# Kernel tuning notes

Measured on AMD Instinct MI355X. Metric: run time of the kernel, lower is better.

Reference implementation:

```python
import jax, jax.numpy as jnp
from jax import lax
import numpy as np

N = 4096      # graph nodes
K = 16        # sampled local-neighborhood size (2-hop proxy)
T = 16        # number of templates
NT = 16       # nodes per template
D = 128       # node feature dim
OUTER = 3     # proximal / mirror-descent iterations
INNER = 5     # sinkhorn iterations per outer step
EPS_REL = 0.1 # entropic reg relative to cost range
TINY = 1e-16


def setup_inputs() -> dict:
    key = jax.random.key(0)
    ks = jax.random.split(key, 8)
    x = jax.random.normal(ks[0], (N, D), jnp.float32)
    adj = (jax.random.uniform(ks[1], (N, N)) < 0.004).astype(jnp.float32)
    adj = jnp.maximum(adj, adj.T)
    neighbors = jax.random.randint(ks[2], (N, K), 0, N, dtype=jnp.int32)
    templates = (jax.random.randint(ks[3], (T, NT, NT), 0, 2).astype(jnp.float32)
                 + 0.01 * jax.random.normal(ks[4], (T, NT, NT), jnp.float32))
    templates_features = 0.0012 + 0.02 * jax.random.normal(ks[5], (T, NT, D), jnp.float32)
    q0 = jax.random.uniform(ks[6], (T, NT), jnp.float32)
    alpha0 = jnp.zeros((1,), jnp.float32)
    return {"x": x, "adj": adj, "neighbors": neighbors, "templates": templates,
            "templates_features": templates_features, "q0": q0, "alpha0": alpha0}


def _ltfgw(x, adj, neighbors, templates, templates_features, q0, alpha0):
    n, d = x.shape
    t, nt, _ = templates.shape
    k1 = neighbors.shape[1] + 1
    nb = jnp.concatenate([jnp.arange(n, dtype=neighbors.dtype)[:, None], neighbors], axis=1)  # [N,K1]
    Fi = x[nb]                                    # [N,K1,D] local node features
    C1 = adj[nb[:, :, None], nb[:, None, :]]      # [N,K1,K1] local structure
    C2 = templates                                # [T,NT,NT]
    alpha = jax.nn.sigmoid(alpha0[0])
    q = jax.nn.softmax(q0, axis=1)                # [T,NT] template node weights
    p = jnp.full((k1,), 1.0 / k1, x.dtype)        # uniform local weights
    # squared-euclidean feature cost M: [N,T,K1,NT]
    M = (jnp.sum(Fi**2, -1)[:, None, :, None]
         + jnp.sum(templates_features**2, -1)[None, :, None, :]
         - 2.0 * jnp.einsum('nkd,tmd->ntkm', Fi, templates_features))
    # constant part of squared-loss GW cost
    cC = (jnp.einsum('nij,j->ni', C1**2, p)[:, None, :, None]
          + jnp.einsum('tm,tlm->tl', q, C2**2)[None, :, None, :])
    G0 = jnp.broadcast_to(p[None, None, :, None] * q[None, :, None, :], (n, t, k1, nt))

    def outer_step(G, _):
        gw_grad = cC - 2.0 * jnp.einsum('nij,ntjm,tlm->ntil', C1, G, C2)
        grad = (1.0 - alpha) * M + alpha * gw_grad
        lo = jnp.min(grad, axis=(-2, -1), keepdims=True)
        hi = jnp.max(grad, axis=(-2, -1), keepdims=True)
        eps = EPS_REL * (hi - lo) + TINY
        Kmat = jnp.exp(-(grad - lo) / eps)        # per-(n,t) shift leaves plan invariant

        def sink(uv, _):
            u, v = uv
            u = p[None, None, :] / jnp.maximum(jnp.einsum('ntkm,ntm->ntk', Kmat, v), TINY)
            v = q[None] / jnp.maximum(jnp.einsum('ntkm,ntk->ntm', Kmat, u), TINY)
            return (u, v), None

        u0 = jnp.ones((n, t, k1), x.dtype)
        v0 = jnp.ones((n, t, nt), x.dtype)
        (u, v), _ = lax.scan(sink, (u0, v0), None, length=INNER)
        return u[..., None] * Kmat * v[..., None, :], None

    G, _ = lax.scan(outer_step, G0, None, length=OUTER)
    gw = cC - 2.0 * jnp.einsum('nij,ntjm,tlm->ntil', C1, G, C2)
    # fused GW distance of every node's local graph to every template: [N,T]
    return jnp.sum(((1.0 - alpha) * M + alpha * gw) * G, axis=(-2, -1))


def reference(x, adj, neighbors, templates, templates_features, q0, alpha0):
    return _ltfgw(x, adj, neighbors, templates, templates_features, q0, alpha0)
```

## Files before the change

### kernel.cpp

```cpp
#include <hip/hip_runtime.h>
#include <math.h>


#define NN 4096
#define KNB 16
#define K1 17
#define C1STRIDE 20
#define C1NODE 340
#define TSTR 296
#define TINYF 1e-16f

typedef const __attribute__((address_space(4))) float* c4fp;
typedef const __attribute__((address_space(4))) int*   c4ip;
__device__ __forceinline__ float sload(const float* p){ return *(c4fp)(unsigned long long)p; }
__device__ __forceinline__ int   sloadi(const int* p) { return *(c4ip)(unsigned long long)p; }

template<int CTRL>
__device__ __forceinline__ float dppmov(float x) {
  return __int_as_float(
      __builtin_amdgcn_update_dpp(0, __float_as_int(x), CTRL, 0xF, 0xF, true));
}
__device__ __forceinline__ float xor4v(float x) {
  return dppmov<0x1B>(dppmov<0x141>(x));
}
__device__ __forceinline__ float rsum16(float x) {
  x += dppmov<0xB1>(x); x += dppmov<0x4E>(x);
  x += xor4v(x);        x += dppmov<0x128>(x);
  return x;
}
__device__ __forceinline__ float rmin16(float x) {
  x = fminf(x, dppmov<0xB1>(x)); x = fminf(x, dppmov<0x4E>(x));
  x = fminf(x, xor4v(x));        x = fminf(x, dppmov<0x128>(x));
  return x;
}
__device__ __forceinline__ float rmax16(float x) {
  x = fmaxf(x, dppmov<0xB1>(x)); x = fmaxf(x, dppmov<0x4E>(x));
  x = fmaxf(x, xor4v(x));        x = fmaxf(x, dppmov<0x128>(x));
  return x;
}
__device__ __forceinline__ float rcpn(float x) {
  float r = __builtin_amdgcn_rcpf(x);
  return r * (2.f - x * r);
}

#define WSTEP(C, R) { g = dppmov<C>(g); acc = fmaf(g, c2reg[R], acc); }
#define WALK15() \
  WSTEP(0xB1,1)  WSTEP(0x1B,2)  WSTEP(0xB1,3)  WSTEP(0x141,4) \
  WSTEP(0xB1,5)  WSTEP(0x1B,6)  WSTEP(0xB1,7)  WSTEP(0x140,8) \
  WSTEP(0xB1,9)  WSTEP(0x1B,10) WSTEP(0xB1,11) WSTEP(0x141,12) \
  WSTEP(0xB1,13) WSTEP(0x1B,14) WSTEP(0xB1,15)

#define PG_GEMM  256
#define PG_XSQ   (PG_GEMM + 1024)
#define PG_SCAL  PG_XSQ
#define PG_C1    (PG_SCAL + 1)
#define PG_TOT   (PG_C1 + 4096)

__global__ __launch_bounds__(256) void prep_combined(
    const float* __restrict__ x, const float* __restrict__ adj,
    const int* __restrict__ neighbors, const float* __restrict__ templates_,
    const float* __restrict__ tf, const float* __restrict__ q0,
    const float* __restrict__ alpha0,
    float* __restrict__ P, float* __restrict__ C1ws, float* __restrict__ xsq,
    float* __restrict__ tfsq, float* __restrict__ qmat, float* __restrict__ cq,
    float* __restrict__ walpha) {
  __shared__ __align__(16) float smem[2 * 64 * 68];
  const int b = blockIdx.x, tid = threadIdx.x;

  if (b < PG_GEMM) {
    float (*As)[68] = (float (*)[68])smem;
    float (*Bs)[68] = (float (*)[68])(smem + 64 * 68);
    int tx = tid & 15, ty = tid >> 4;
    int r0 = (b & 63) * 64, c0 = (b >> 6) * 64;
    float acc[4][4] = {};
    for (int h = 0; h < 2; ++h) {
      __syncthreads();
#pragma unroll
      for (int q = 0; q < 4; ++q) {
        int f = tid + 256*q;
        int row = f >> 4, d4 = (f & 15) << 2;
        float4 a = *(const float4*)&x[(r0+row)*128 + h*64 + d4];
        As[d4+0][row]=a.x; As[d4+1][row]=a.y; As[d4+2][row]=a.z; As[d4+3][row]=a.w;
        float4 bb = *(const float4*)&tf[(c0+row)*128 + h*64 + d4];
        Bs[d4+0][row]=bb.x; Bs[d4+1][row]=bb.y; Bs[d4+2][row]=bb.z; Bs[d4+3][row]=bb.w;
      }
      __syncthreads();
#pragma unroll
      for (int d = 0; d < 64; ++d) {
        float4 a = *(const float4*)&As[d][ty*4];
        float4 bb = *(const float4*)&Bs[d][tx*4];
        float av[4]={a.x,a.y,a.z,a.w}, bv[4]={bb.x,bb.y,bb.z,bb.w};
#pragma unroll
        for (int i = 0; i < 4; ++i)
#pragma unroll
          for (int j = 0; j < 4; ++j) acc[i][j] = fmaf(av[i], bv[j], acc[i][j]);
      }
    }
#pragma unroll
    for (int i = 0; i < 4; ++i) {
      float4 o; o.x=acc[i][0]; o.y=acc[i][1]; o.z=acc[i][2]; o.w=acc[i][3];
      *(float4*)&P[(r0 + ty*4 + i)*256 + c0 + tx*4] = o;
    }
    return;
  }

  if (b < PG_XSQ) {
    int n = (b - PG_GEMM)*4 + (tid >> 6), lane = tid & 63;
    float2 v = *(const float2*)&x[n*128 + lane*2];
    float s = fmaf(v.x, v.x, v.y*v.y);
    s += __shfl_xor(s,1); s += __shfl_xor(s,2);  s += __shfl_xor(s,4);
    s += __shfl_xor(s,8); s += __shfl_xor(s,16); s += __shfl_xor(s,32);
    if (lane == 0) xsq[n] = s;
    return;
  }

  if (b == PG_SCAL) {
    int t = tid >> 4, l = tid & 15;
    if (tid == 0) walpha[0] = 1.f / (1.f + expf(-alpha0[0]));
    float qr[16]; float mx = -3.0e38f;
#pragma unroll
    for (int m = 0; m < 16; ++m) { qr[m] = q0[t*16+m]; mx = fmaxf(mx, qr[m]); }
    float s = 0.f;
#pragma unroll
    for (int m = 0; m < 16; ++m) { qr[m] = expf(qr[m]-mx); s += qr[m]; }
    float inv = 1.f / s;
    qmat[tid] = qr[l] * inv;
    float c = 0.f;
#pragma unroll
    for (int m = 0; m < 16; ++m) {
      float c2 = templates_[t*256 + l*16 + m];
      c = fmaf(qr[m]*inv, c2*c2, c);
    }
    cq[tid] = c;
    float ts = 0.f;
#pragma unroll
    for (int dq = 0; dq < 32; ++dq) {
      float4 v = *(const float4*)&tf[tid*128 + dq*4];
      ts = fmaf(v.x,v.x,ts); ts = fmaf(v.y,v.y,ts);
      ts = fmaf(v.z,v.z,ts); ts = fmaf(v.w,v.w,ts);
    }
    tfsq[tid] = ts;
    return;
  }

  {
    int n = b - PG_C1;
    int*   nbs  = (int*)smem;
    float* c1sh = smem + 32;
    if (tid < K1) nbs[tid] = (tid == 0) ? n : neighbors[n*KNB + tid - 1];
    __syncthreads();
    for (int e = tid; e < 289; e += 256) {
      int i = e / 17, j = e % 17;
      float v = adj[nbs[i]*NN + nbs[j]];
      C1ws[n*C1NODE + i*C1STRIDE + j] = v;
      c1sh[e] = v;
    }
    __syncthreads();
    bool nz = false;
    if (tid < K1) {
      float s = 0.f;
#pragma unroll
      for (int j = 0; j < K1; ++j) {
        float v = c1sh[tid*17 + j];
        s = fmaf(v, v, s); nz |= (v != 0.f);
      }
      C1ws[n*C1NODE + tid*C1STRIDE + 17] = s * (1.f/17.f);
    }
    unsigned long long bal = __ballot(nz);
    if (tid == 0)
      ((int*)C1ws)[n*C1NODE + 18] = (int)(bal & 0x1FFFF);
  }
}

__global__ __launch_bounds__(256, 2) void ltfgw_main(
    const float* __restrict__ P, const float* __restrict__ C1ws,
    const float* __restrict__ xsq, const float* __restrict__ tfsq,
    const float* __restrict__ qmat, const float* __restrict__ cq,
    const float* __restrict__ walpha, const int* __restrict__ neighbors,
    const float* __restrict__ templates_, float* __restrict__ out) {
  __shared__ __align__(16) float Ksh[16 * TSTR];
  __shared__ __align__(16) float Ush[256];
  __shared__ __align__(16) float Vsh[256];

  const int tid = threadIdx.x;
  const int t = tid >> 4, l = tid & 15;
  const int n = blockIdx.x;

  const float alpha = sload(walpha);
  const float oma = 1.f - alpha;
  const float na2 = -2.f * alpha;
  const int mask = sloadi((const int*)C1ws + n*C1NODE + 18);

  int nbk[K1];
  nbk[0] = n;
#pragma unroll
  for (int k = 1; k < K1; ++k) nbk[k] = sloadi(neighbors + n*KNB + (k-1));

  const float tfsq_l = tfsq[tid];
  const float cq_l   = cq[tid];
  const float q_l    = qmat[tid];

  float Mcol[K1];
#pragma unroll
  for (int k = 0; k < K1; ++k) {
    float xs  = sload(xsq + nbk[k]);
    float cc1 = sload(C1ws + n*C1NODE + k*C1STRIDE + 17);
    float pv  = P[nbk[k]*256 + tid];
    Mcol[k] = oma * (xs + tfsq_l - 2.f*pv) + alpha * (cc1 + cq_l);
  }

  float c2reg[16];
#pragma unroll
  for (int r = 0; r < 16; ++r)
    c2reg[r] = na2 * templates_[t*256 + l*16 + (l ^ r)];

  float Gcol[K1];
#pragma unroll
  for (int j = 0; j < K1; ++j) Gcol[j] = (1.f/17.f) * q_l;

  const int tb = t * TSTR;
  float ur[16], u16 = 0.f, vm = 1.f;

#pragma unroll 1
  for (int outer = 0; outer < 3; ++outer) {
    float Kc[K1];
    float lo = 3.0e38f, hi = -3.0e38f;
#pragma unroll
    for (int i = 0; i < K1; ++i) {
      float gr = Mcol[i];
      if (mask & (1 << i)) {
        const float* c1r = C1ws + n*C1NODE + i*C1STRIDE;
        float s = 0.f;
#pragma unroll
        for (int j = 0; j < K1; ++j) s = fmaf(sload(c1r + j), Gcol[j], s);
        float g = s, acc = s * c2reg[0];
        WALK15()
        gr += acc;
      }
      Kc[i] = gr;
      lo = fminf(lo, gr); hi = fmaxf(hi, gr);
    }
    lo = rmin16(lo); hi = rmax16(hi);
    float eps = 0.1f * (hi - lo) + TINYF;
    float sc = 1.4426950408889634f * __builtin_amdgcn_rcpf(eps);
    float nsc = -sc, losc = lo * sc;
#pragma unroll
    for (int i = 0; i < K1; ++i) {
      Kc[i] = __builtin_amdgcn_exp2f(fmaf(Kc[i], nsc, losc));
      Ksh[tb + i*17 + l] = Kc[i];
    }
    float Krow[16];
#pragma unroll
    for (int jq = 0; jq < 4; ++jq) {
      float4 v = *(const float4*)&Ksh[tb + l*17 + jq*4];
      Krow[jq*4+0]=v.x; Krow[jq*4+1]=v.y; Krow[jq*4+2]=v.z; Krow[jq*4+3]=v.w;
    }

    float vlane = 1.f;
    Vsh[tid] = 1.f;
#pragma unroll 1
    for (int it = 0; it < 5; ++it) {
      float vr[16];
#pragma unroll
      for (int q = 0; q < 4; ++q) {
        float4 v = *(const float4*)&Vsh[t*16 + q*4];
        vr[q*4+0]=v.x; vr[q*4+1]=v.y; vr[q*4+2]=v.z; vr[q*4+3]=v.w;
      }
      float w = 0.f;
#pragma unroll
      for (int j = 0; j < 16; ++j) w = fmaf(Krow[j], vr[j], w);
      float w16 = rsum16(Kc[16] * vlane);
      float um = (1.f/17.f) * rcpn(fmaxf(w,   TINYF));
      u16      = (1.f/17.f) * rcpn(fmaxf(w16, TINYF));
      Ush[tid] = um;
#pragma unroll
      for (int q = 0; q < 4; ++q) {
        float4 v = *(const float4*)&Ush[t*16 + q*4];
        ur[q*4+0]=v.x; ur[q*4+1]=v.y; ur[q*4+2]=v.z; ur[q*4+3]=v.w;
      }
      float sg = u16 * Kc[16];
#pragma unroll
      for (int k = 0; k < 16; ++k) sg = fmaf(ur[k], Kc[k], sg);
      vlane = q_l * rcpn(fmaxf(sg, TINYF));
      Vsh[tid] = vlane;
    }
    vm = vlane;
#pragma unroll
    for (int k = 0; k < 16; ++k) Gcol[k] = ur[k] * Kc[k] * vm;
    Gcol[16] = u16 * Kc[16] * vm;
  }

  float acc1 = 0.f;
#pragma unroll
  for (int i = 0; i < K1; ++i) acc1 = fmaf(Mcol[i], Gcol[i], acc1);
#pragma unroll
  for (int i = 0; i < K1; ++i) {
    if (mask & (1 << i)) {
      const float* c1r = C1ws + n*C1NODE + i*C1STRIDE;
      float s = 0.f;
#pragma unroll
      for (int j = 0; j < K1; ++j) s = fmaf(sload(c1r + j), Gcol[j], s);
      float g = s, acc = s * c2reg[0];
      WALK15()
      acc1 = fmaf(acc, Gcol[i], acc1);
    }
  }
  float accout = rsum16(acc1);
  if (l == 0) out[n*16 + t] = accout;
}

extern "C" void kernel_launch(void* const* d_in, const int* in_sizes, int n_in,
                              void* d_out, int out_size, void* d_ws, size_t ws_size,
                              hipStream_t stream) {
  const float* x          = (const float*)d_in[0];
  const float* adj        = (const float*)d_in[1];
  const int*   neighbors  = (const int*)  d_in[2];
  const float* templates_ = (const float*)d_in[3];
  const float* tfeat      = (const float*)d_in[4];
  const float* q0         = (const float*)d_in[5];
  const float* alpha0     = (const float*)d_in[6];
  float* out = (float*)d_out;

  float* ws     = (float*)d_ws;
  float* P      = ws;
  float* C1ws   = P + 4096*256;
  float* xsq    = C1ws + 4096*C1NODE;
  float* tfsq   = xsq + 4096;
  float* qmat   = tfsq + 256;
  float* cq     = qmat + 256;
  float* walpha = cq + 256;

  hipLaunchKernelGGL(prep_combined, dim3(PG_TOT), dim3(256), 0, stream,
                     x, adj, neighbors, templates_, tfeat, q0, alpha0,
                     P, C1ws, xsq, tfsq, qmat, cq, walpha);
  hipLaunchKernelGGL(ltfgw_main, dim3(4096), dim3(256), 0, stream,
                     P, C1ws, xsq, tfsq, qmat, cq, walpha, neighbors,
                     templates_, out);
}
```

Baseline: 181.1 us.

## Bit-pack adjacency matrix and gather local structure from packed bits

Adds a streaming pass that converts the dense float adjacency into a bitmask via wave ballots. The per-node C1 gather now runs as a separate kernel that reads bits instead of scattered floats. The intent is to replace latency-bound random reads of a 64 MB matrix with one coalesced sweep plus cache-friendly gathers from an 8x smaller array. It adds a kernel launch and a full read of adj. The exp argument is also computed with a sub/mul instead of a precomputed FMA.

```diff
diff --git a/kernel.cpp b/kernel.cpp
--- a/kernel.cpp
+++ b/kernel.cpp
@@ -51,18 +51,18 @@
   WSTEP(0xB1,13) WSTEP(0x1B,14) WSTEP(0xB1,15)
 
 #define PG_GEMM  256
-#define PG_XSQ   (PG_GEMM + 1024)
+#define PG_PACK  (PG_GEMM + 1024)
+#define PG_XSQ   (PG_PACK + 1024)
 #define PG_SCAL  PG_XSQ
-#define PG_C1    (PG_SCAL + 1)
-#define PG_TOT   (PG_C1 + 4096)
+#define PG_TOT   (PG_SCAL + 1)
 
 __global__ __launch_bounds__(256) void prep_combined(
     const float* __restrict__ x, const float* __restrict__ adj,
-    const int* __restrict__ neighbors, const float* __restrict__ templates_,
-    const float* __restrict__ tf, const float* __restrict__ q0,
-    const float* __restrict__ alpha0,
-    float* __restrict__ P, float* __restrict__ C1ws, float* __restrict__ xsq,
-    float* __restrict__ tfsq, float* __restrict__ qmat, float* __restrict__ cq,
+    const float* __restrict__ templates_, const float* __restrict__ tf,
+    const float* __restrict__ q0, const float* __restrict__ alpha0,
+    float* __restrict__ P, unsigned long long* __restrict__ pk,
+    float* __restrict__ xsq, float* __restrict__ tfsq,
+    float* __restrict__ qmat, float* __restrict__ cq,
     float* __restrict__ walpha) {
   __shared__ __align__(16) float smem[2 * 64 * 68];
   const int b = blockIdx.x, tid = threadIdx.x;
@@ -104,8 +104,21 @@
     return;
   }
 
+  if (b < PG_PACK) {
+    int wave = (b - PG_GEMM)*4 + (tid >> 6);
+    int lane = tid & 63;
+#pragma unroll 4
+    for (int it = 0; it < 64; ++it) {
+      int w64 = wave + it*4096;
+      float v = adj[(size_t)w64*64 + lane];
+      unsigned long long m = __ballot(v != 0.f);
+      if (lane == 0) pk[w64] = m;
+    }
+    return;
+  }
+
   if (b < PG_XSQ) {
-    int n = (b - PG_GEMM)*4 + (tid >> 6), lane = tid & 63;
+    int n = (b - PG_PACK)*4 + (tid >> 6), lane = tid & 63;
     float2 v = *(const float2*)&x[n*128 + lane*2];
     float s = fmaf(v.x, v.x, v.y*v.y);
     s += __shfl_xor(s,1); s += __shfl_xor(s,2);  s += __shfl_xor(s,4);
@@ -114,7 +127,7 @@
     return;
   }
 
-  if (b == PG_SCAL) {
+  {
     int t = tid >> 4, l = tid & 15;
     if (tid == 0) walpha[0] = 1.f / (1.f + expf(-alpha0[0]));
     float qr[16]; float mx = -3.0e38f;
@@ -140,36 +153,40 @@
       ts = fmaf(v.z,v.z,ts); ts = fmaf(v.w,v.w,ts);
     }
     tfsq[tid] = ts;
-    return;
-  }
-
-  {
-    int n = b - PG_C1;
-    int*   nbs  = (int*)smem;
-    float* c1sh = smem + 32;
-    if (tid < K1) nbs[tid] = (tid == 0) ? n : neighbors[n*KNB + tid - 1];
-    __syncthreads();
-    for (int e = tid; e < 289; e += 256) {
-      int i = e / 17, j = e % 17;
-      float v = adj[nbs[i]*NN + nbs[j]];
-      C1ws[n*C1NODE + i*C1STRIDE + j] = v;
-      c1sh[e] = v;
-    }
-    __syncthreads();
-    bool nz = false;
-    if (tid < K1) {
-      float s = 0.f;
-#pragma unroll
-      for (int j = 0; j < K1; ++j) {
-        float v = c1sh[tid*17 + j];
-        s = fmaf(v, v, s); nz |= (v != 0.f);
-      }
-      C1ws[n*C1NODE + tid*C1STRIDE + 17] = s * (1.f/17.f);
-    }
-    unsigned long long bal = __ballot(nz);
-    if (tid == 0)
-      ((int*)C1ws)[n*C1NODE + 18] = (int)(bal & 0x1FFFF);
-  }
+  }
+}
+
+__global__ __launch_bounds__(256) void c1gather_packed(
+    const unsigned* __restrict__ pku, const int* __restrict__ neighbors,
+    float* __restrict__ C1ws) {
+  __shared__ int nbs[K1];
+  __shared__ float c1sh[K1 * K1];
+  int n = blockIdx.x;
+  int tid = threadIdx.x;
+  if (tid < K1) nbs[tid] = (tid == 0) ? n : neighbors[n*KNB + tid - 1];
+  __syncthreads();
+  for (int e = tid; e < 289; e += 256) {
+    int i = e / 17, j = e % 17;
+    int col = nbs[j];
+    unsigned w = pku[nbs[i]*128 + (col >> 5)];
+    float v = ((w >> (col & 31)) & 1u) ? 1.f : 0.f;
+    C1ws[n*C1NODE + i*C1STRIDE + j] = v;
+    c1sh[e] = v;
+  }
+  __syncthreads();
+  bool nz = false;
+  if (tid < K1) {
+    float s = 0.f;
+#pragma unroll
+    for (int j = 0; j < K1; ++j) {
+      float v = c1sh[tid*17 + j];
+      s = fmaf(v, v, s); nz |= (v != 0.f);
+    }
+    C1ws[n*C1NODE + tid*C1STRIDE + 17] = s * (1.f/17.f);
+  }
+  unsigned long long bal = __ballot(nz);
+  if (tid == 0)
+    ((int*)C1ws)[n*C1NODE + 18] = (int)(bal & 0x1FFFF);
 }
 
 __global__ __launch_bounds__(256, 2) void ltfgw_main(
@@ -243,10 +260,9 @@
     lo = rmin16(lo); hi = rmax16(hi);
     float eps = 0.1f * (hi - lo) + TINYF;
     float sc = 1.4426950408889634f * __builtin_amdgcn_rcpf(eps);
-    float nsc = -sc, losc = lo * sc;
 #pragma unroll
     for (int i = 0; i < K1; ++i) {
-      Kc[i] = __builtin_amdgcn_exp2f(fmaf(Kc[i], nsc, losc));
+      Kc[i] = __builtin_amdgcn_exp2f((lo - Kc[i]) * sc);
       Ksh[tb + i*17 + l] = Kc[i];
     }
     float Krow[16];
@@ -329,10 +345,13 @@
   float* qmat   = tfsq + 256;
   float* cq     = qmat + 256;
   float* walpha = cq + 256;
+  unsigned long long* pk = (unsigned long long*)(walpha + 8);
 
   hipLaunchKernelGGL(prep_combined, dim3(PG_TOT), dim3(256), 0, stream,
-                     x, adj, neighbors, templates_, tfeat, q0, alpha0,
-                     P, C1ws, xsq, tfsq, qmat, cq, walpha);
+                     x, adj, templates_, tfeat, q0, alpha0,
+                     P, pk, xsq, tfsq, qmat, cq, walpha);
+  hipLaunchKernelGGL(c1gather_packed, dim3(4096), dim3(256), 0, stream,
+                     (const unsigned*)pk, neighbors, C1ws);
   hipLaunchKernelGGL(ltfgw_main, dim3(4096), dim3(256), 0, stream,
                      P, C1ws, xsq, tfsq, qmat, cq, walpha, neighbors,
                      templates_, out);
```

Measured after the change: 198.7 us. 1.1x slower.

## Replace LDS-based Sinkhorn exchange with DPP xor-walk register reductions

Applied to the files above, without the earlier changes.

The Sinkhorn inner loop no longer passes u and v between lanes through shared memory each iteration. Each lane loads its K row and column in xor-permuted order once, then computes both matvecs with a DPP lane walk, and the loop is fully unrolled with the first iteration specialised for v=1. This removes per-iteration LDS writes and reads and their implied waits, at the cost of more DPP moves and higher register pressure from the extra 32 permuted K values. It also widens the adjacency index to size_t and slightly reorders the exp argument arithmetic.

```diff
diff --git a/kernel.cpp b/kernel.cpp
--- a/kernel.cpp
+++ b/kernel.cpp
@@ -20,6 +20,18 @@
   return __int_as_float(
       __builtin_amdgcn_update_dpp(0, __float_as_int(x), CTRL, 0xF, 0xF, true));
 }
+template<int M> __device__ __forceinline__ float quadx(float x) {
+  if constexpr (M==0) return x;
+  else if constexpr (M==1) return dppmov<0xB1>(x);
+  else if constexpr (M==2) return dppmov<0x4E>(x);
+  else return dppmov<0x1B>(x);
+}
+template<int R> __device__ __forceinline__ float xorperm(float x) {
+  if constexpr (R < 4)       return quadx<R>(x);
+  else if constexpr (R < 8)  return quadx<R^7>(dppmov<0x141>(x));
+  else if constexpr (R < 12) return quadx<R^8>(dppmov<0x128>(x));
+  else                       return quadx<R^15>(dppmov<0x140>(x));
+}
 __device__ __forceinline__ float xor4v(float x) {
   return dppmov<0x1B>(dppmov<0x141>(x));
 }
@@ -43,12 +55,12 @@
   return r * (2.f - x * r);
 }
 
-#define WSTEP(C, R) { g = dppmov<C>(g); acc = fmaf(g, c2reg[R], acc); }
-#define WALK15() \
-  WSTEP(0xB1,1)  WSTEP(0x1B,2)  WSTEP(0xB1,3)  WSTEP(0x141,4) \
-  WSTEP(0xB1,5)  WSTEP(0x1B,6)  WSTEP(0xB1,7)  WSTEP(0x140,8) \
-  WSTEP(0xB1,9)  WSTEP(0x1B,10) WSTEP(0xB1,11) WSTEP(0x141,12) \
-  WSTEP(0xB1,13) WSTEP(0x1B,14) WSTEP(0xB1,15)
+#define WSTEPA(C, R, A) { g = dppmov<C>(g); acc = fmaf(g, A[R], acc); }
+#define WALKA(A) \
+  WSTEPA(0xB1,1,A)  WSTEPA(0x1B,2,A)  WSTEPA(0xB1,3,A)  WSTEPA(0x141,4,A) \
+  WSTEPA(0xB1,5,A)  WSTEPA(0x1B,6,A)  WSTEPA(0xB1,7,A)  WSTEPA(0x140,8,A) \
+  WSTEPA(0xB1,9,A)  WSTEPA(0x1B,10,A) WSTEPA(0xB1,11,A) WSTEPA(0x141,12,A) \
+  WSTEPA(0xB1,13,A) WSTEPA(0x1B,14,A) WSTEPA(0xB1,15,A)
 
 #define PG_GEMM  256
 #define PG_XSQ   (PG_GEMM + 1024)
@@ -151,7 +163,7 @@
     __syncthreads();
     for (int e = tid; e < 289; e += 256) {
       int i = e / 17, j = e % 17;
-      float v = adj[nbs[i]*NN + nbs[j]];
+      float v = adj[(size_t)nbs[i]*NN + nbs[j]];
       C1ws[n*C1NODE + i*C1STRIDE + j] = v;
       c1sh[e] = v;
     }
@@ -180,7 +192,6 @@
     const float* __restrict__ templates_, float* __restrict__ out) {
   __shared__ __align__(16) float Ksh[16 * TSTR];
   __shared__ __align__(16) float Ush[256];
-  __shared__ __align__(16) float Vsh[256];
 
   const int tid = threadIdx.x;
   const int t = tid >> 4, l = tid & 15;
@@ -219,7 +230,6 @@
   for (int j = 0; j < K1; ++j) Gcol[j] = (1.f/17.f) * q_l;
 
   const int tb = t * TSTR;
-  float ur[16], u16 = 0.f, vm = 1.f;
 
 #pragma unroll 1
   for (int outer = 0; outer < 3; ++outer) {
@@ -234,7 +244,7 @@
 #pragma unroll
         for (int j = 0; j < K1; ++j) s = fmaf(sload(c1r + j), Gcol[j], s);
         float g = s, acc = s * c2reg[0];
-        WALK15()
+        WALKA(c2reg)
         gr += acc;
       }
       Kc[i] = gr;
@@ -243,51 +253,64 @@
     lo = rmin16(lo); hi = rmax16(hi);
     float eps = 0.1f * (hi - lo) + TINYF;
     float sc = 1.4426950408889634f * __builtin_amdgcn_rcpf(eps);
-    float nsc = -sc, losc = lo * sc;
 #pragma unroll
     for (int i = 0; i < K1; ++i) {
-      Kc[i] = __builtin_amdgcn_exp2f(fmaf(Kc[i], nsc, losc));
+      Kc[i] = __builtin_amdgcn_exp2f((lo - Kc[i]) * sc);
       Ksh[tb + i*17 + l] = Kc[i];
     }
-    float Krow[16];
-#pragma unroll
-    for (int jq = 0; jq < 4; ++jq) {
-      float4 v = *(const float4*)&Ksh[tb + l*17 + jq*4];
-      Krow[jq*4+0]=v.x; Krow[jq*4+1]=v.y; Krow[jq*4+2]=v.z; Krow[jq*4+3]=v.w;
-    }
-
-    float vlane = 1.f;
-    Vsh[tid] = 1.f;
-#pragma unroll 1
-    for (int it = 0; it < 5; ++it) {
-      float vr[16];
-#pragma unroll
-      for (int q = 0; q < 4; ++q) {
-        float4 v = *(const float4*)&Vsh[t*16 + q*4];
-        vr[q*4+0]=v.x; vr[q*4+1]=v.y; vr[q*4+2]=v.z; vr[q*4+3]=v.w;
-      }
-      float w = 0.f;
-#pragma unroll
-      for (int j = 0; j < 16; ++j) w = fmaf(Krow[j], vr[j], w);
-      float w16 = rsum16(Kc[16] * vlane);
-      float um = (1.f/17.f) * rcpn(fmaxf(w,   TINYF));
-      u16      = (1.f/17.f) * rcpn(fmaxf(w16, TINYF));
-      Ush[tid] = um;
-#pragma unroll
-      for (int q = 0; q < 4; ++q) {
-        float4 v = *(const float4*)&Ush[t*16 + q*4];
-        ur[q*4+0]=v.x; ur[q*4+1]=v.y; ur[q*4+2]=v.z; ur[q*4+3]=v.w;
-      }
-      float sg = u16 * Kc[16];
-#pragma unroll
-      for (int k = 0; k < 16; ++k) sg = fmaf(ur[k], Kc[k], sg);
-      vlane = q_l * rcpn(fmaxf(sg, TINYF));
-      Vsh[tid] = vlane;
-    }
-    vm = vlane;
-#pragma unroll
-    for (int k = 0; k < 16; ++k) Gcol[k] = ur[k] * Kc[k] * vm;
-    Gcol[16] = u16 * Kc[16] * vm;
+    const float Kc16 = Kc[16];
+
+    float Krp[16], Kcp[16];
+#pragma unroll
+    for (int r = 0; r < 16; ++r) Krp[r] = Ksh[tb + l*17 + (l ^ r)];
+    Kcp[0] = Krp[0];
+    Kcp[1]=xorperm<1>(Krp[1]);    Kcp[2]=xorperm<2>(Krp[2]);
+    Kcp[3]=xorperm<3>(Krp[3]);    Kcp[4]=xorperm<4>(Krp[4]);
+    Kcp[5]=xorperm<5>(Krp[5]);    Kcp[6]=xorperm<6>(Krp[6]);
+    Kcp[7]=xorperm<7>(Krp[7]);    Kcp[8]=xorperm<8>(Krp[8]);
+    Kcp[9]=xorperm<9>(Krp[9]);    Kcp[10]=xorperm<10>(Krp[10]);
+    Kcp[11]=xorperm<11>(Krp[11]); Kcp[12]=xorperm<12>(Krp[12]);
+    Kcp[13]=xorperm<13>(Krp[13]); Kcp[14]=xorperm<14>(Krp[14]);
+    Kcp[15]=xorperm<15>(Krp[15]);
+
+    float uloc, u16, vcur;
+    {
+      float acc = Krp[0];
+#pragma unroll
+      for (int r = 1; r < 16; ++r) acc += Krp[r];
+      float w16 = rsum16(Kc16);
+      uloc = (1.f/17.f) * rcpn(fmaxf(acc, TINYF));
+      u16  = (1.f/17.f) * rcpn(fmaxf(w16, TINYF));
+      float g = uloc;
+      acc = fmaf(u16, Kc16, g * Kcp[0]);
+      WALKA(Kcp)
+      vcur = q_l * rcpn(fmaxf(acc, TINYF));
+    }
+#pragma unroll
+    for (int it = 1; it < 5; ++it) {
+      float g = vcur;
+      float acc = g * Krp[0];
+      WALKA(Krp)
+      float w16 = rsum16(Kc16 * vcur);
+      uloc = (1.f/17.f) * rcpn(fmaxf(acc, TINYF));
+      u16  = (1.f/17.f) * rcpn(fmaxf(w16, TINYF));
+      g = uloc;
+      acc = fmaf(u16, Kc16, g * Kcp[0]);
+      WALKA(Kcp)
+      vcur = q_l * rcpn(fmaxf(acc, TINYF));
+    }
+    const float vm = vcur;
+
+    Ush[tid] = uloc;
+#pragma unroll
+    for (int q = 0; q < 4; ++q) {
+      float4 uv = *(const float4*)&Ush[t*16 + q*4];
+      Gcol[q*4+0] = Kc[q*4+0] * uv.x * vm;
+      Gcol[q*4+1] = Kc[q*4+1] * uv.y * vm;
+      Gcol[q*4+2] = Kc[q*4+2] * uv.z * vm;
+      Gcol[q*4+3] = Kc[q*4+3] * uv.w * vm;
+    }
+    Gcol[16] = Kc16 * u16 * vm;
   }
 
   float acc1 = 0.f;
@@ -301,7 +324,7 @@
 #pragma unroll
       for (int j = 0; j < K1; ++j) s = fmaf(sload(c1r + j), Gcol[j], s);
       float g = s, acc = s * c2reg[0];
-      WALK15()
+      WALKA(c2reg)
       acc1 = fmaf(acc, Gcol[i], acc1);
     }
   }
```

Measured after the change: 197.2 us. 1.09x slower.
